# Kernel tuning notes

Measured on AMD Instinct MI355X. Metric: run time of the kernel, lower is better.

The kernel has to match this reference:

```python
import jax, jax.numpy as jnp
import numpy as np

TWO_PI = 6.283185307179586


def setup_inputs() -> dict:
    key = jax.random.key(0)
    k1, k2, k3, k4, k5, k6 = jax.random.split(key, 6)
    B, T, D = 2, 8192, 1024
    x = jax.random.normal(k1, (B, T, D), dtype=jnp.float32)
    # nn.Linear weights are [out, in]; init with small scale like torch default
    s = 1.0 / np.sqrt(D)
    Wk = jax.random.uniform(k2, (D, D), jnp.float32, -s, s)
    Wv = jax.random.uniform(k3, (D, D), jnp.float32, -s, s)
    Wo = jax.random.uniform(k4, (D, D), jnp.float32, -s, s)
    # random phasor frequencies in [0, 2*pi)
    freqs = jax.random.uniform(k5, (D,), jnp.float32, 0.0, TWO_PI)
    return {"x": x, "Wk": Wk, "Wv": Wv, "Wo": Wo, "freqs": freqs}


def reference(x, Wk, Wv, Wo, freqs):
    B, T, C = x.shape
    # k projection is computed in the original forward but never used downstream
    k_real = x @ Wk.T  # [B,T,D] (dead value, kept for fidelity)
    v_real = x @ Wv.T  # [B,T,D]
    v = v_real.astype(jnp.complex64)
    # rotors: per-position unit phasors exp(i * t * freqs), shape [T, D]
    t = jnp.arange(T, dtype=jnp.float32)
    rotors = jnp.exp(1j * (t[:, None] * freqs[None, :])).astype(jnp.complex64)
    # bind each value with its rotor and accumulate causally (O(N) memory trace)
    memory_trace = jnp.cumsum(v * rotors[None, :, :], axis=1)  # [B,T,D] complex64
    # retrieve by unbinding with the conjugate rotor; take the real component
    retrieved = jnp.real(memory_trace * jnp.conj(rotors)[None, :, :])  # [B,T,D]
    return retrieved @ Wo.T
```

## Files before the change

kernel.cpp:

```cpp
#include <hip/hip_runtime.h>
#include <hip/hip_bf16.h>


#define B_  2
#define T_  8192
#define D_  1024
#define BT_ 16384
#define CS_ 32
#define NCHUNK_ 256

typedef __attribute__((ext_vector_type(4))) float f32x4;
typedef __attribute__((ext_vector_type(8))) short bf16x8;

static __device__ inline unsigned short f2bf(float f) {
    union { float f; unsigned int u; } a;
    a.f = f;
    unsigned int u = a.u;
    return (unsigned short)((u + 0x7FFFu + ((u >> 16) & 1u)) >> 16);
}
static __device__ inline float bf2f(unsigned short h) {
    union { unsigned int u; float f; } a;
    a.u = ((unsigned int)h) << 16;
    return a.f;
}
static __device__ inline int fsw(int r) { return ((r & 3) + ((r >> 2) & 3)) & 3; }

__global__ __launch_bounds__(256) void cast_all(const float* __restrict__ x,
                                                const float* __restrict__ Wv,
                                                const float* __restrict__ Wo,
                                                unsigned short* __restrict__ xb,
                                                unsigned short* __restrict__ wvb,
                                                unsigned short* __restrict__ wob) {
    const int nx = BT_ * D_ / 4;
    const int nw = D_ * D_ / 4;
    int i = blockIdx.x * 256 + threadIdx.x;
    const float4* src;
    unsigned short* dst;
    int j;
    if (i < nx)            { src = (const float4*)x;  dst = xb;  j = i; }
    else if (i < nx + nw)  { src = (const float4*)Wv; dst = wvb; j = i - nx; }
    else                   { src = (const float4*)Wo; dst = wob; j = i - nx - nw; }
    float4 v = src[j];
    ushort4 o;
    o.x = f2bf(v.x); o.y = f2bf(v.y); o.z = f2bf(v.z); o.w = f2bf(v.w);
    ((ushort4*)dst)[j] = o;
}

template <bool BF16OUT>
__global__ __launch_bounds__(256) void gemm_bt(const short* __restrict__ A,
                                               const short* __restrict__ Bm,
                                               void* __restrict__ Cout,
                                               int M, int N, int K) {
    __shared__ short lds[8192];
    const int lane = threadIdx.x & 63;
    const int wave = threadIdx.x >> 6;
    const int wr = wave >> 1, wc = wave & 1;

    const int nb = N >> 7;
    const int id = blockIdx.x;
    const int xcd = id & 7;
    const int slot = id >> 3;
    const int bn = (slot % nb) * 128;
    const int bm = (xcd * ((M >> 7) >> 3) + slot / nb) * 128;

    const int r0 = lane >> 2;
    const int cb = lane & 3;

    const short* ga[2];
    const short* gb[2];
#pragma unroll
    for (int cc = 0; cc < 2; ++cc) {
        const int chunk = wave * 2 + cc;
        const int row = chunk * 16 + r0;
        const int col = (cb ^ fsw(row)) * 8;
        ga[cc] = A + (size_t)(bm + row) * K + col;
        gb[cc] = Bm + (size_t)(bn + row) * K + col;
    }

    const int c4r = lane >> 4;
    int aoff[4], boff[4];
#pragma unroll
    for (int i = 0; i < 4; ++i) {
        const int m = wr * 64 + (lane & 15) + i * 16;
        aoff[i] = m * 32 + ((c4r ^ fsw(m)) * 8);
        const int n = wc * 64 + (lane & 15) + i * 16;
        boff[i] = 4096 + n * 32 + ((c4r ^ fsw(n)) * 8);
    }

    f32x4 acc[4][4] = {};

    for (int k0 = 0; k0 < K; k0 += 32) {
#pragma unroll
        for (int cc = 0; cc < 2; ++cc) {
            const int chunk = wave * 2 + cc;
            __builtin_amdgcn_global_load_lds(
                (const __attribute__((address_space(1))) void*)(ga[cc] + k0),
                (__attribute__((address_space(3))) void*)&lds[chunk * 512], 16, 0, 0);
            __builtin_amdgcn_global_load_lds(
                (const __attribute__((address_space(1))) void*)(gb[cc] + k0),
                (__attribute__((address_space(3))) void*)&lds[4096 + chunk * 512], 16, 0, 0);
        }
        __syncthreads();
        bf16x8 a[4], b[4];
#pragma unroll
        for (int i = 0; i < 4; ++i) a[i] = *(const bf16x8*)&lds[aoff[i]];
#pragma unroll
        for (int j = 0; j < 4; ++j) b[j] = *(const bf16x8*)&lds[boff[j]];
#pragma unroll
        for (int i = 0; i < 4; ++i)
#pragma unroll
            for (int j = 0; j < 4; ++j)
                acc[i][j] = __builtin_amdgcn_mfma_f32_16x16x32_bf16(a[i], b[j], acc[i][j], 0, 0, 0);
        __syncthreads();
    }

    const int row0 = (lane >> 4) * 4;
#pragma unroll
    for (int i = 0; i < 4; ++i) {
#pragma unroll
        for (int j = 0; j < 4; ++j) {
            const int col = bn + wc * 64 + j * 16 + (lane & 15);
#pragma unroll
            for (int r = 0; r < 4; ++r) {
                const size_t row = bm + wr * 64 + i * 16 + row0 + r;
                if constexpr (BF16OUT)
                    ((unsigned short*)Cout)[row * N + col] = f2bf(acc[i][j][r]);
                else
                    ((float*)Cout)[row * N + col] = acc[i][j][r];
            }
        }
    }
}

__global__ __launch_bounds__(256) void scan_pass1(const unsigned short* __restrict__ v,
                                                  const float* __restrict__ freqs,
                                                  float* __restrict__ csum) {
    const int tid = threadIdx.x;
    const int chunk = blockIdx.x * 2 + (tid >> 7);
    const int b = blockIdx.y;
    const int d0 = (tid & 127) * 8;

    float fr[8], s[8], c[8], sf[8], cf[8], ar[8] = {}, ai[8] = {};
    {
        float4 fA = *(const float4*)(freqs + d0);
        float4 fB = *(const float4*)(freqs + d0 + 4);
        fr[0] = fA.x; fr[1] = fA.y; fr[2] = fA.z; fr[3] = fA.w;
        fr[4] = fB.x; fr[5] = fB.y; fr[6] = fB.z; fr[7] = fB.w;
    }
    const float t0f = (float)(chunk * CS_);
#pragma unroll
    for (int k = 0; k < 8; ++k) {
        sincosf(t0f * fr[k], &s[k], &c[k]);
        sincosf(fr[k], &sf[k], &cf[k]);
    }
    const uint4* vp = (const uint4*)(v + ((size_t)b * T_ + chunk * CS_) * D_ + d0);
    for (int tb = 0; tb < CS_; tb += 8) {
        uint4 w[8];
#pragma unroll
        for (int u = 0; u < 8; ++u) w[u] = vp[(size_t)(tb + u) * (D_ / 8)];
#pragma unroll
        for (int u = 0; u < 8; ++u) {
            const unsigned int wd[4] = {w[u].x, w[u].y, w[u].z, w[u].w};
#pragma unroll
            for (int k = 0; k < 8; ++k) {
                float wv = bf2f((unsigned short)(wd[k >> 1] >> ((k & 1) * 16)));
                ar[k] = fmaf(wv, c[k], ar[k]);
                ai[k] = fmaf(wv, s[k], ai[k]);
                float nc = c[k] * cf[k] - s[k] * sf[k];
                float ns = s[k] * cf[k] + c[k] * sf[k];
                c[k] = nc; s[k] = ns;
            }
        }
    }
    float4* cp = (float4*)(csum + (((size_t)b * NCHUNK_ + chunk) * D_ + d0) * 2);
#pragma unroll
    for (int k = 0; k < 4; ++k) {
        float4 o; o.x = ar[2 * k]; o.y = ai[2 * k]; o.z = ar[2 * k + 1]; o.w = ai[2 * k + 1];
        cp[k] = o;
    }
}

__global__ __launch_bounds__(256) void scan_pass2(float* __restrict__ csum) {
    const int g = blockIdx.x * 256 + threadIdx.x;
    const int b = g / D_;
    const int d = g % D_;
    float2* cs = (float2*)csum;
    const size_t base = (size_t)b * NCHUNK_ * D_ + d;
    float pr = 0.f, pi = 0.f;
    for (int cc = 0; cc < NCHUNK_; cc += 16) {
        float2 buf[16];
#pragma unroll
        for (int k = 0; k < 16; ++k) buf[k] = cs[base + (size_t)(cc + k) * D_];
#pragma unroll
        for (int k = 0; k < 16; ++k) {
            float r = buf[k].x, im = buf[k].y;
            buf[k] = make_float2(pr, pi);
            pr += r; pi += im;
        }
#pragma unroll
        for (int k = 0; k < 16; ++k) cs[base + (size_t)(cc + k) * D_] = buf[k];
    }
}

__global__ __launch_bounds__(256) void scan_pass3(const unsigned short* __restrict__ v,
                                                  const float* __restrict__ freqs,
                                                  const float* __restrict__ csum,
                                                  unsigned short* __restrict__ ret) {
    const int tid = threadIdx.x;
    const int chunk = blockIdx.x * 2 + (tid >> 7);
    const int b = blockIdx.y;
    const int d0 = (tid & 127) * 8;

    float fr[8], s[8], c[8], sf[8], cf[8], ar[8], ai[8];
    {
        float4 fA = *(const float4*)(freqs + d0);
        float4 fB = *(const float4*)(freqs + d0 + 4);
        fr[0] = fA.x; fr[1] = fA.y; fr[2] = fA.z; fr[3] = fA.w;
        fr[4] = fB.x; fr[5] = fB.y; fr[6] = fB.z; fr[7] = fB.w;
    }
    const float t0f = (float)(chunk * CS_);
#pragma unroll
    for (int k = 0; k < 8; ++k) {
        sincosf(t0f * fr[k], &s[k], &c[k]);
        sincosf(fr[k], &sf[k], &cf[k]);
    }
    {
        const float4* cp = (const float4*)(csum + (((size_t)b * NCHUNK_ + chunk) * D_ + d0) * 2);
#pragma unroll
        for (int k = 0; k < 4; ++k) {
            float4 o = cp[k];
            ar[2 * k] = o.x; ai[2 * k] = o.y; ar[2 * k + 1] = o.z; ai[2 * k + 1] = o.w;
        }
    }
    const uint4* vp = (const uint4*)(v + ((size_t)b * T_ + chunk * CS_) * D_ + d0);
    uint4* rp = (uint4*)(ret + ((size_t)b * T_ + chunk * CS_) * D_ + d0);
    for (int tb = 0; tb < CS_; tb += 8) {
        uint4 w[8];
#pragma unroll
        for (int u = 0; u < 8; ++u) w[u] = vp[(size_t)(tb + u) * (D_ / 8)];
#pragma unroll
        for (int u = 0; u < 8; ++u) {
            const unsigned int wd[4] = {w[u].x, w[u].y, w[u].z, w[u].w};
            unsigned int od[4];
#pragma unroll
            for (int k = 0; k < 8; k += 2) {
                float w0 = bf2f((unsigned short)(wd[k >> 1]));
                float w1 = bf2f((unsigned short)(wd[k >> 1] >> 16));
                ar[k] = fmaf(w0, c[k], ar[k]); ai[k] = fmaf(w0, s[k], ai[k]);
                ar[k + 1] = fmaf(w1, c[k + 1], ar[k + 1]); ai[k + 1] = fmaf(w1, s[k + 1], ai[k + 1]);
                float o0 = ar[k] * c[k] + ai[k] * s[k];
                float o1 = ar[k + 1] * c[k + 1] + ai[k + 1] * s[k + 1];
                od[k >> 1] = (unsigned int)f2bf(o0) | ((unsigned int)f2bf(o1) << 16);
#pragma unroll
                for (int q = 0; q < 2; ++q) {
                    float nc = c[k + q] * cf[k + q] - s[k + q] * sf[k + q];
                    float ns = s[k + q] * cf[k + q] + c[k + q] * sf[k + q];
                    c[k + q] = nc; s[k + q] = ns;
                }
            }
            uint4 o4; o4.x = od[0]; o4.y = od[1]; o4.z = od[2]; o4.w = od[3];
            rp[(size_t)(tb + u) * (D_ / 8)] = o4;
        }
    }
}

extern "C" void kernel_launch(void* const* d_in, const int* in_sizes, int n_in,
                              void* d_out, int out_size, void* d_ws, size_t ws_size,
                              hipStream_t stream) {
    const float* x     = (const float*)d_in[0];
    const float* Wv    = (const float*)d_in[2];
    const float* Wo    = (const float*)d_in[3];
    const float* freqs = (const float*)d_in[4];
    float* out = (float*)d_out;

    char* ws = (char*)d_ws;
    unsigned short* x_bf  = (unsigned short*)ws;
    unsigned short* Wv_bf = (unsigned short*)(ws + 33554432);
    unsigned short* Wo_bf = (unsigned short*)(ws + 35651584);
    unsigned short* ret   = (unsigned short*)(ws + 37748736);
    float*          csum  = (float*)(ws + 71303168);
    unsigned short* v_bf = (unsigned short*)d_out;

    cast_all<<<(BT_ * D_ / 4 + 2 * D_ * D_ / 4) / 256, 256, 0, stream>>>(
        x, Wv, Wo, x_bf, Wv_bf, Wo_bf);

    gemm_bt<true><<<(BT_ / 128) * (D_ / 128), 256, 0, stream>>>(
        (const short*)x_bf, (const short*)Wv_bf, (void*)v_bf, BT_, D_, D_);

    dim3 sgrid(NCHUNK_ / 2, B_);
    scan_pass1<<<sgrid, 256, 0, stream>>>(v_bf, freqs, csum);
    scan_pass2<<<(B_ * D_) / 256, 256, 0, stream>>>(csum);
    scan_pass3<<<sgrid, 256, 0, stream>>>(v_bf, freqs, csum, ret);

    gemm_bt<false><<<(BT_ / 128) * (D_ / 128), 256, 0, stream>>>(
        (const short*)ret, (const short*)Wo_bf, (void*)out, BT_, D_, D_);
}
```

Measured before the change: 282.0 us.

## Double GEMM K-tile to 64 with 8-way XOR swizzle; narrow scan per-thread width

The GEMM now stages a K=64 slice per iteration, with an 8-column XOR swizzle in a doubled LDS buffer. This halves the number of barrier pairs and global-to-LDS round trips per output tile, at the cost of more LDS per block. The scan passes now handle 4 channels per thread instead of 8, with one chunk per block and twice as many blocks, to raise parallelism and reduce register pressure. Pass 2 buffers 32 chunks per load batch instead of 16.

```diff
diff --git a/kernel.cpp b/kernel.cpp
--- a/kernel.cpp
+++ b/kernel.cpp
@@ -23,7 +23,6 @@
     a.u = ((unsigned int)h) << 16;
     return a.f;
 }
-static __device__ inline int fsw(int r) { return ((r & 3) + ((r >> 2) & 3)) & 3; }
 
 __global__ __launch_bounds__(256) void cast_all(const float* __restrict__ x,
                                                 const float* __restrict__ Wv,
@@ -51,7 +50,7 @@
                                                const short* __restrict__ Bm,
                                                void* __restrict__ Cout,
                                                int M, int N, int K) {
-    __shared__ short lds[8192];
+    __shared__ short lds[16384];
     const int lane = threadIdx.x & 63;
     const int wave = threadIdx.x >> 6;
     const int wr = wave >> 1, wc = wave & 1;
@@ -63,54 +62,59 @@
     const int bn = (slot % nb) * 128;
     const int bm = (xcd * ((M >> 7) >> 3) + slot / nb) * 128;
 
-    const int r0 = lane >> 2;
-    const int cb = lane & 3;
-
-    const short* ga[2];
-    const short* gb[2];
-#pragma unroll
-    for (int cc = 0; cc < 2; ++cc) {
-        const int chunk = wave * 2 + cc;
-        const int row = chunk * 16 + r0;
-        const int col = (cb ^ fsw(row)) * 8;
+    const int sr = lane >> 3;
+    const int cb = lane & 7;
+    const short* ga[4];
+    const short* gb[4];
+#pragma unroll
+    for (int cc = 0; cc < 4; ++cc) {
+        const int chunk = wave * 4 + cc;
+        const int row = chunk * 8 + sr;
+        const int col = (cb ^ (row & 7)) * 8;
         ga[cc] = A + (size_t)(bm + row) * K + col;
         gb[cc] = Bm + (size_t)(bn + row) * K + col;
     }
 
     const int c4r = lane >> 4;
-    int aoff[4], boff[4];
+    int aoff[4][2], boff[4][2];
 #pragma unroll
     for (int i = 0; i < 4; ++i) {
         const int m = wr * 64 + (lane & 15) + i * 16;
-        aoff[i] = m * 32 + ((c4r ^ fsw(m)) * 8);
         const int n = wc * 64 + (lane & 15) + i * 16;
-        boff[i] = 4096 + n * 32 + ((c4r ^ fsw(n)) * 8);
+#pragma unroll
+        for (int ks = 0; ks < 2; ++ks) {
+            aoff[i][ks] = m * 64 + (((ks * 4 + c4r) ^ (m & 7)) * 8);
+            boff[i][ks] = 8192 + n * 64 + (((ks * 4 + c4r) ^ (n & 7)) * 8);
+        }
     }
 
     f32x4 acc[4][4] = {};
 
-    for (int k0 = 0; k0 < K; k0 += 32) {
-#pragma unroll
-        for (int cc = 0; cc < 2; ++cc) {
-            const int chunk = wave * 2 + cc;
+    for (int k0 = 0; k0 < K; k0 += 64) {
+#pragma unroll
+        for (int cc = 0; cc < 4; ++cc) {
+            const int chunk = wave * 4 + cc;
             __builtin_amdgcn_global_load_lds(
                 (const __attribute__((address_space(1))) void*)(ga[cc] + k0),
                 (__attribute__((address_space(3))) void*)&lds[chunk * 512], 16, 0, 0);
             __builtin_amdgcn_global_load_lds(
                 (const __attribute__((address_space(1))) void*)(gb[cc] + k0),
-                (__attribute__((address_space(3))) void*)&lds[4096 + chunk * 512], 16, 0, 0);
+                (__attribute__((address_space(3))) void*)&lds[8192 + chunk * 512], 16, 0, 0);
         }
         __syncthreads();
-        bf16x8 a[4], b[4];
-#pragma unroll
-        for (int i = 0; i < 4; ++i) a[i] = *(const bf16x8*)&lds[aoff[i]];
-#pragma unroll
-        for (int j = 0; j < 4; ++j) b[j] = *(const bf16x8*)&lds[boff[j]];
-#pragma unroll
-        for (int i = 0; i < 4; ++i)
-#pragma unroll
-            for (int j = 0; j < 4; ++j)
-                acc[i][j] = __builtin_amdgcn_mfma_f32_16x16x32_bf16(a[i], b[j], acc[i][j], 0, 0, 0);
+#pragma unroll
+        for (int ks = 0; ks < 2; ++ks) {
+            bf16x8 a[4], b[4];
+#pragma unroll
+            for (int i = 0; i < 4; ++i) a[i] = *(const bf16x8*)&lds[aoff[i][ks]];
+#pragma unroll
+            for (int j = 0; j < 4; ++j) b[j] = *(const bf16x8*)&lds[boff[j][ks]];
+#pragma unroll
+            for (int i = 0; i < 4; ++i)
+#pragma unroll
+                for (int j = 0; j < 4; ++j)
+                    acc[i][j] = __builtin_amdgcn_mfma_f32_16x16x32_bf16(a[i], b[j], acc[i][j], 0, 0, 0);
+        }
         __syncthreads();
     }
 
@@ -135,37 +139,37 @@
 __global__ __launch_bounds__(256) void scan_pass1(const unsigned short* __restrict__ v,
                                                   const float* __restrict__ freqs,
                                                   float* __restrict__ csum) {
-    const int tid = threadIdx.x;
-    const int chunk = blockIdx.x * 2 + (tid >> 7);
+    const int d0 = threadIdx.x * 4;
+    const int chunk = blockIdx.x;
     const int b = blockIdx.y;
-    const int d0 = (tid & 127) * 8;
-
-    float fr[8], s[8], c[8], sf[8], cf[8], ar[8] = {}, ai[8] = {};
+
+    float fr[4], s[4], c[4], sf[4], cf[4], ar[4] = {}, ai[4] = {};
     {
-        float4 fA = *(const float4*)(freqs + d0);
-        float4 fB = *(const float4*)(freqs + d0 + 4);
-        fr[0] = fA.x; fr[1] = fA.y; fr[2] = fA.z; fr[3] = fA.w;
-        fr[4] = fB.x; fr[5] = fB.y; fr[6] = fB.z; fr[7] = fB.w;
+        float4 f4 = *(const float4*)(freqs + d0);
+        fr[0] = f4.x; fr[1] = f4.y; fr[2] = f4.z; fr[3] = f4.w;
     }
     const float t0f = (float)(chunk * CS_);
 #pragma unroll
-    for (int k = 0; k < 8; ++k) {
+    for (int k = 0; k < 4; ++k) {
         sincosf(t0f * fr[k], &s[k], &c[k]);
         sincosf(fr[k], &sf[k], &cf[k]);
     }
-    const uint4* vp = (const uint4*)(v + ((size_t)b * T_ + chunk * CS_) * D_ + d0);
+    const uint2* vp = (const uint2*)(v + ((size_t)b * T_ + chunk * CS_) * D_ + d0);
     for (int tb = 0; tb < CS_; tb += 8) {
-        uint4 w[8];
-#pragma unroll
-        for (int u = 0; u < 8; ++u) w[u] = vp[(size_t)(tb + u) * (D_ / 8)];
+        uint2 w[8];
+#pragma unroll
+        for (int u = 0; u < 8; ++u) w[u] = vp[(size_t)(tb + u) * (D_ / 4)];
 #pragma unroll
         for (int u = 0; u < 8; ++u) {
-            const unsigned int wd[4] = {w[u].x, w[u].y, w[u].z, w[u].w};
-#pragma unroll
-            for (int k = 0; k < 8; ++k) {
-                float wv = bf2f((unsigned short)(wd[k >> 1] >> ((k & 1) * 16)));
-                ar[k] = fmaf(wv, c[k], ar[k]);
-                ai[k] = fmaf(wv, s[k], ai[k]);
+            float wv[4];
+            wv[0] = bf2f((unsigned short)w[u].x);
+            wv[1] = bf2f((unsigned short)(w[u].x >> 16));
+            wv[2] = bf2f((unsigned short)w[u].y);
+            wv[3] = bf2f((unsigned short)(w[u].y >> 16));
+#pragma unroll
+            for (int k = 0; k < 4; ++k) {
+                ar[k] = fmaf(wv[k], c[k], ar[k]);
+                ai[k] = fmaf(wv[k], s[k], ai[k]);
                 float nc = c[k] * cf[k] - s[k] * sf[k];
                 float ns = s[k] * cf[k] + c[k] * sf[k];
                 c[k] = nc; s[k] = ns;
@@ -173,11 +177,10 @@
         }
     }
     float4* cp = (float4*)(csum + (((size_t)b * NCHUNK_ + chunk) * D_ + d0) * 2);
-#pragma unroll
-    for (int k = 0; k < 4; ++k) {
-        float4 o; o.x = ar[2 * k]; o.y = ai[2 * k]; o.z = ar[2 * k + 1]; o.w = ai[2 * k + 1];
-        cp[k] = o;
-    }
+    float4 o0, o1;
+    o0.x = ar[0]; o0.y = ai[0]; o0.z = ar[1]; o0.w = ai[1];
+    o1.x = ar[2]; o1.y = ai[2]; o1.z = ar[3]; o1.w = ai[3];
+    cp[0] = o0; cp[1] = o1;
 }
 
 __global__ __launch_bounds__(256) void scan_pass2(float* __restrict__ csum) {
@@ -187,18 +190,18 @@
     float2* cs = (float2*)csum;
     const size_t base = (size_t)b * NCHUNK_ * D_ + d;
     float pr = 0.f, pi = 0.f;
-    for (int cc = 0; cc < NCHUNK_; cc += 16) {
-        float2 buf[16];
-#pragma unroll
-        for (int k = 0; k < 16; ++k) buf[k] = cs[base + (size_t)(cc + k) * D_];
-#pragma unroll
-        for (int k = 0; k < 16; ++k) {
+    for (int cc = 0; cc < NCHUNK_; cc += 32) {
+        float2 buf[32];
+#pragma unroll
+        for (int k = 0; k < 32; ++k) buf[k] = cs[base + (size_t)(cc + k) * D_];
+#pragma unroll
+        for (int k = 0; k < 32; ++k) {
             float r = buf[k].x, im = buf[k].y;
             buf[k] = make_float2(pr, pi);
             pr += r; pi += im;
         }
 #pragma unroll
-        for (int k = 0; k < 16; ++k) cs[base + (size_t)(cc + k) * D_] = buf[k];
+        for (int k = 0; k < 32; ++k) cs[base + (size_t)(cc + k) * D_] = buf[k];
     }
 }
 
@@ -206,60 +209,53 @@
                                                   const float* __restrict__ freqs,
                                                   const float* __restrict__ csum,
                                                   unsigned short* __restrict__ ret) {
-    const int tid = threadIdx.x;
-    const int chunk = blockIdx.x * 2 + (tid >> 7);
+    const int d0 = threadIdx.x * 4;
+    const int chunk = blockIdx.x;
     const int b = blockIdx.y;
-    const int d0 = (tid & 127) * 8;
-
-    float fr[8], s[8], c[8], sf[8], cf[8], ar[8], ai[8];
+
+    float fr[4], s[4], c[4], sf[4], cf[4], ar[4], ai[4];
     {
-        float4 fA = *(const float4*)(freqs + d0);
-        float4 fB = *(const float4*)(freqs + d0 + 4);
-        fr[0] = fA.x; fr[1] = fA.y; fr[2] = fA.z; fr[3] = fA.w;
-        fr[4] = fB.x; fr[5] = fB.y; fr[6] = fB.z; fr[7] = fB.w;
+        float4 f4 = *(const float4*)(freqs + d0);
+        fr[0] = f4.x; fr[1] = f4.y; fr[2] = f4.z; fr[3] = f4.w;
     }
     const float t0f = (float)(chunk * CS_);
 #pragma unroll
-    for (int k = 0; k < 8; ++k) {
+    for (int k = 0; k < 4; ++k) {
         sincosf(t0f * fr[k], &s[k], &c[k]);
         sincosf(fr[k], &sf[k], &cf[k]);
     }
     {
         const float4* cp = (const float4*)(csum + (((size_t)b * NCHUNK_ + chunk) * D_ + d0) * 2);
-#pragma unroll
-        for (int k = 0; k < 4; ++k) {
-            float4 o = cp[k];
-            ar[2 * k] = o.x; ai[2 * k] = o.y; ar[2 * k + 1] = o.z; ai[2 * k + 1] = o.w;
-        }
-    }
-    const uint4* vp = (const uint4*)(v + ((size_t)b * T_ + chunk * CS_) * D_ + d0);
-    uint4* rp = (uint4*)(ret + ((size_t)b * T_ + chunk * CS_) * D_ + d0);
+        float4 o0 = cp[0], o1 = cp[1];
+        ar[0] = o0.x; ai[0] = o0.y; ar[1] = o0.z; ai[1] = o0.w;
+        ar[2] = o1.x; ai[2] = o1.y; ar[3] = o1.z; ai[3] = o1.w;
+    }
+    const uint2* vp = (const uint2*)(v + ((size_t)b * T_ + chunk * CS_) * D_ + d0);
+    uint2* rp = (uint2*)(ret + ((size_t)b * T_ + chunk * CS_) * D_ + d0);
     for (int tb = 0; tb < CS_; tb += 8) {
-        uint4 w[8];
-#pragma unroll
-        for (int u = 0; u < 8; ++u) w[u] = vp[(size_t)(tb + u) * (D_ / 8)];
+        uint2 w[8];
+#pragma unroll
+        for (int u = 0; u < 8; ++u) w[u] = vp[(size_t)(tb + u) * (D_ / 4)];
 #pragma unroll
         for (int u = 0; u < 8; ++u) {
-            const unsigned int wd[4] = {w[u].x, w[u].y, w[u].z, w[u].w};
-            unsigned int od[4];
-#pragma unroll
-            for (int k = 0; k < 8; k += 2) {
-                float w0 = bf2f((unsigned short)(wd[k >> 1]));
-                float w1 = bf2f((unsigned short)(wd[k >> 1] >> 16));
-                ar[k] = fmaf(w0, c[k], ar[k]); ai[k] = fmaf(w0, s[k], ai[k]);
-                ar[k + 1] = fmaf(w1, c[k + 1], ar[k + 1]); ai[k + 1] = fmaf(w1, s[k + 1], ai[k + 1]);
-                float o0 = ar[k] * c[k] + ai[k] * s[k];
-                float o1 = ar[k + 1] * c[k + 1] + ai[k + 1] * s[k + 1];
-                od[k >> 1] = (unsigned int)f2bf(o0) | ((unsigned int)f2bf(o1) << 16);
-#pragma unroll
-                for (int q = 0; q < 2; ++q) {
-                    float nc = c[k + q] * cf[k + q] - s[k + q] * sf[k + q];
-                    float ns = s[k + q] * cf[k + q] + c[k + q] * sf[k + q];
-                    c[k + q] = nc; s[k + q] = ns;
-                }
+            float wv[4], o[4];
+            wv[0] = bf2f((unsigned short)w[u].x);
+            wv[1] = bf2f((unsigned short)(w[u].x >> 16));
+            wv[2] = bf2f((unsigned short)w[u].y);
+            wv[3] = bf2f((unsigned short)(w[u].y >> 16));
+#pragma unroll
+            for (int k = 0; k < 4; ++k) {
+                ar[k] = fmaf(wv[k], c[k], ar[k]);
+                ai[k] = fmaf(wv[k], s[k], ai[k]);
+                o[k] = ar[k] * c[k] + ai[k] * s[k];
+                float nc = c[k] * cf[k] - s[k] * sf[k];
+                float ns = s[k] * cf[k] + c[k] * sf[k];
+                c[k] = nc; s[k] = ns;
             }
-            uint4 o4; o4.x = od[0]; o4.y = od[1]; o4.z = od[2]; o4.w = od[3];
-            rp[(size_t)(tb + u) * (D_ / 8)] = o4;
+            uint2 o2;
+            o2.x = (unsigned int)f2bf(o[0]) | ((unsigned int)f2bf(o[1]) << 16);
+            o2.y = (unsigned int)f2bf(o[2]) | ((unsigned int)f2bf(o[3]) << 16);
+            rp[(size_t)(tb + u) * (D_ / 4)] = o2;
         }
     }
 }
@@ -287,7 +283,7 @@
     gemm_bt<true><<<(BT_ / 128) * (D_ / 128), 256, 0, stream>>>(
         (const short*)x_bf, (const short*)Wv_bf, (void*)v_bf, BT_, D_, D_);
 
-    dim3 sgrid(NCHUNK_ / 2, B_);
+    dim3 sgrid(NCHUNK_, B_);
     scan_pass1<<<sgrid, 256, 0, stream>>>(v_bf, freqs, csum);
     scan_pass2<<<(B_ * D_) / 256, 256, 0, stream>>>(csum);
     scan_pass3<<<sgrid, 256, 0, stream>>>(v_bf, freqs, csum, ret);
```

Result: faster. 257.3 us (-8.7%).
